# Performance work log

Measured on AMD Instinct MI355X. Metric: run time of the kernel, lower is better.

## Reference

```python
import jax, jax.numpy as jnp
import numpy as np

NTYPES = 2
NATOMS = (512, 512)
N = 1024          # total atoms
NN = 128          # neighbors per type
M = NTYPES * NN   # 256 neighbor slots per atom
D = 25            # last embedding width
FH = 240          # fitting hidden width
B = 8
RMIN, RMAX = 5.8, 6.0


def _embed_mlp(s, W0, b0, W1, b1, W2, b2):
    # DeepMD-style resnet embedding net: 1 -> D -> D -> D, tanh + skip
    h = jnp.tanh(s @ W0 + b0)
    h = h + jnp.tanh(h @ W1 + b1)
    h = h + jnp.tanh(h @ W2 + b2)
    return h


def setup_inputs() -> dict:
    key = jax.random.key(0)
    ks = jax.random.split(key, 20)
    # relative positions; components in [-4.5, 4.5] so |r| spans <5.8, [5.8,6.0), >=6.0
    image_dR = (jax.random.uniform(ks[0], (B, N, NTYPES, NN, 3), jnp.float32) - 0.5) * 9.0
    # 0 == empty neighbor slot (mask = list_neigh > 0); index-1 in [0, N)
    list_neigh = jax.random.randint(ks[1], (B, N, NTYPES, NN), 0, 1025)
    davg = 0.1 * jax.random.normal(ks[2], (NTYPES, M, 4), jnp.float32)
    dstd = jax.random.uniform(ks[3], (NTYPES, M, 4), jnp.float32, 0.5, 1.5)
    P = NTYPES * NTYPES
    eW0 = jax.random.normal(ks[4], (P, 1, D), jnp.float32)
    eb0 = 0.1 * jax.random.normal(ks[5], (P, D), jnp.float32)
    eW1 = jax.random.normal(ks[6], (P, D, D), jnp.float32) / np.sqrt(D)
    eb1 = 0.1 * jax.random.normal(ks[7], (P, D), jnp.float32)
    eW2 = jax.random.normal(ks[8], (P, D, D), jnp.float32) / np.sqrt(D)
    eb2 = 0.1 * jax.random.normal(ks[9], (P, D), jnp.float32)
    fW0 = jax.random.normal(ks[10], (NTYPES, 16 * D, FH), jnp.float32) / np.sqrt(16 * D)
    fb0 = 0.1 * jax.random.normal(ks[11], (NTYPES, FH), jnp.float32)
    fW1 = jax.random.normal(ks[12], (NTYPES, FH, FH), jnp.float32) / np.sqrt(FH)
    fb1 = 0.1 * jax.random.normal(ks[13], (NTYPES, FH), jnp.float32)
    fW2 = jax.random.normal(ks[14], (NTYPES, FH, FH), jnp.float32) / np.sqrt(FH)
    fb2 = 0.1 * jax.random.normal(ks[15], (NTYPES, FH), jnp.float32)
    fW3 = jax.random.normal(ks[16], (NTYPES, FH, 1), jnp.float32) / np.sqrt(FH)
    fb3 = 0.1 * jax.random.normal(ks[17], (NTYPES, 1), jnp.float32)
    ener_shift = 0.01 * jax.random.normal(ks[18], (NTYPES,), jnp.float32)
    return {
        'image_dR': image_dR, 'list_neigh': list_neigh,
        'davg': davg, 'dstd': dstd,
        'eW0': eW0, 'eb0': eb0, 'eW1': eW1, 'eb1': eb1, 'eW2': eW2, 'eb2': eb2,
        'fW0': fW0, 'fb0': fb0, 'fW1': fW1, 'fb1': fb1, 'fW2': fW2, 'fb2': fb2,
        'fW3': fW3, 'fb3': fb3, 'ener_shift': ener_shift,
        'dfeat': jnp.zeros((1,), jnp.float32),
        'Egroup_weight': jnp.zeros((1,), jnp.float32),
        'divider': jnp.ones((1,), jnp.float32),
    }


def _forward(image_dR, list_neigh, davg, dstd,
             eW0, eb0, eW1, eb1, eW2, eb2,
             fW0, fb0, fW1, fb1, fW2, fb2, fW3, fb3, ener_shift):
    dR = image_dR.reshape(B, N, M, 3)
    neigh = list_neigh.reshape(B, N, M)
    mask = neigh > 0
    mf = mask.astype(dR.dtype)
    dR2 = jnp.sum(dR * dR, axis=-1)                       # [B,N,M]
    safe_dR2 = jnp.where(mask, dR2, 1.0)
    Rij = jnp.sqrt(safe_dR2)
    inr = mf / Rij                                        # 1/|r|, 0 off-mask
    x = Rij * mf                                          # nr = dR2/Rij = |r|
    Ri_xyz = dR / safe_dR2[..., None] * mf[..., None]     # r / |r|^2
    inr2 = inr * inr
    inr4 = inr2 * inr2
    inr3 = inr4 * x
    # smooth switching function on [RMIN, RMAX]
    u = (x - RMIN) / (RMAX - RMIN)
    poly = u * u * u * (-6.0 * u * u + 15.0 * u - 10.0) + 1.0
    dpoly = (3.0 * u * u * (-6.0 * u * u + 15.0 * u - 10.0)
             + u * u * u * (-12.0 * u + 15.0)) / (RMAX - RMIN)
    mid = (x >= RMIN) & (x < RMAX)
    vv = jnp.where(x < RMIN, 1.0, jnp.where(mid, poly, 0.0)) * mf
    dvv = jnp.where(mid, dpoly, 0.0) * mf
    Ri_pre = jnp.concatenate([inr[..., None], Ri_xyz], axis=-1)   # [B,N,M,4]
    common = (dvv * inr)[..., None] * dR                          # [B,N,M,3]
    row0 = dR * (inr3 * vv)[..., None] - Ri_pre[..., 0:1] * common
    eye = jnp.eye(3, dtype=dR.dtype)
    outer = (2.0 * dR[..., :, None] * dR[..., None, :] * inr4[..., None, None]
             - eye * inr2[..., None, None])                       # [B,N,M,3,3]
    rows = outer * vv[..., None, None] - Ri_pre[..., 1:4, None] * common[..., None, :]
    Ri_d = jnp.concatenate([row0[..., None, :], rows], axis=-2) * mf[..., None, None]  # [B,N,M,4,3]
    Ri = Ri_pre * vv[..., None]
    # per-type normalization stats broadcast over atoms of each type
    davg_res = jnp.concatenate([jnp.broadcast_to(davg[t], (NATOMS[t], M, 4)) for t in range(NTYPES)], axis=0)
    dstd_res = jnp.concatenate([jnp.broadcast_to(dstd[t], (NATOMS[t], M, 4)) for t in range(NTYPES)], axis=0)
    Ri = (Ri - davg_res) / dstd_res
    Ri_d = Ri_d / dstd_res[..., None]

    def ei_fn(Ri_n):
        Ei_list = []
        start = 0
        for t in range(NTYPES):
            na = NATOMS[t]
            Rt = jax.lax.slice_in_dim(Ri_n, start, start + na, axis=1)  # [B,na,M,4]
            acc = jnp.zeros((B, na, 4, D), Ri_n.dtype)
            for t1 in range(NTYPES):
                p = t * NTYPES + t1
                blk = Rt[:, :, t1 * NN:(t1 + 1) * NN]                  # [B,na,NN,4]
                G = _embed_mlp(blk[..., 0:1], eW0[p], eb0[p], eW1[p], eb1[p], eW2[p], eb2[p])
                acc = acc + jnp.einsum('bnkd,bnke->bnde', blk, G)
            acc = acc * (4.0 / (NN * NTYPES * 4))
            DRt = jnp.einsum('bnde,bndf->bnef', acc, acc[..., :16]).reshape(B, na, D * 16)
            h = jnp.tanh(DRt @ fW0[t] + fb0[t])
            h = h + jnp.tanh(h @ fW1[t] + fb1[t])
            h = h + jnp.tanh(h @ fW2[t] + fb2[t])
            Ei_list.append(h @ fW3[t] + fb3[t] + ener_shift[t])
            start += na
        return jnp.concatenate(Ei_list, axis=1)   # [B,N,1]

    Ei, vjpf = jax.vjp(ei_fn, Ri)
    dE, = vjpf(jnp.ones_like(Ei))                 # dEi/dRi  [B,N,M,4]
    Etot = jnp.sum(Ei, axis=1)                    # [B,1]
    pair = jnp.einsum('bnmd,bnmdx->bnmx', dE, Ri_d)   # per-pair force term [B,N,M,3]
    F_self = -jnp.sum(pair, axis=2)
    j = neigh - 1
    valid = j >= 0
    flat_idx = jnp.where(valid, j, N) + jnp.arange(B)[:, None, None] * (N + 1)
    contrib = jnp.where(valid[..., None], pair, 0.0)
    seg = jax.ops.segment_sum(contrib.reshape(-1, 3), flat_idx.reshape(-1), num_segments=B * (N + 1))
    F = F_self + seg.reshape(B, N + 1, 3)[:, :N]
    return Etot, Ei, F


def reference(image_dR, list_neigh, davg, dstd,
              eW0, eb0, eW1, eb1, eW2, eb2,
              fW0, fb0, fW1, fb1, fW2, fb2, fW3, fb3, ener_shift,
              dfeat, Egroup_weight, divider):
    # dfeat / Egroup_weight / divider are in the torch forward signature but unused
    return _forward(image_dR, list_neigh, davg, dstd,
                    eW0, eb0, eW1, eb1, eW2, eb2,
                    fW0, fb0, fW1, fb1, fW2, fb2, fW3, fb3, ener_shift)
```

## Files before the change

kernel.cpp:

```cpp
#include <hip/hip_runtime.h>

#define DEV __device__ __forceinline__

namespace {

constexpr int B_ = 8;
constexpr int N_ = 1024;
constexpr int M_ = 256;
constexpr int D_ = 25;
constexpr int FH_ = 240;
constexpr int NATOM = B_ * N_;
constexpr float CSC = 1.0f / 256.0f;

DEV float fast_tanh(float x) {
  float ax = fabsf(x);
  float e = __expf(-2.0f * ax);
  float r = (1.0f - e) * __builtin_amdgcn_rcpf(1.0f + e);
  return copysignf(r, x);
}

template <bool WANT_RID>
DEV void compute_geom(float dx, float dy, float dz, int nb, int t, int m,
                      const float* __restrict__ davg, const float* __restrict__ dstd,
                      float* __restrict__ blk, float* __restrict__ rid) {
  float mf = (nb > 0) ? 1.0f : 0.0f;
  float dr2 = dx * dx + dy * dy + dz * dz;
  float safe = (nb > 0) ? dr2 : 1.0f;
  float rs = __builtin_amdgcn_rsqf(safe);
  float rij = safe * rs;
  float inr = mf * rs;
  float x = rij * mf;
  float inr2 = inr * inr;
  float inr4 = inr2 * inr2;
  float inr3 = inr4 * x;
  float u = (x - 5.8f) * 5.0f;
  float uu = u * u;
  float A = -6.0f * uu + 15.0f * u - 10.0f;
  float poly = uu * u * A + 1.0f;
  float dpoly = (3.0f * uu * A + uu * u * (-12.0f * u + 15.0f)) * 5.0f;
  bool mid = (x >= 5.8f) && (x < 6.0f);
  float vv = ((x < 5.8f) ? 1.0f : (mid ? poly : 0.0f)) * mf;
  float dvv = (mid ? dpoly : 0.0f) * mf;
  float pre[4];
  pre[0] = inr;
  pre[1] = dx * inr2;
  pre[2] = dy * inr2;
  pre[3] = dz * inr2;
  int bidx = (t * M_ + m) * 4;
  float4 av = *(const float4*)(davg + bidx);
  float4 sv = *(const float4*)(dstd + bidx);
  float avf[4] = {av.x, av.y, av.z, av.w};
  float rsv[4] = {__builtin_amdgcn_rcpf(sv.x), __builtin_amdgcn_rcpf(sv.y),
                  __builtin_amdgcn_rcpf(sv.z), __builtin_amdgcn_rcpf(sv.w)};
#pragma unroll
  for (int d = 0; d < 4; ++d) blk[d] = (pre[d] * vv - avf[d]) * rsv[d];
  if (WANT_RID) {
    float dv[3] = {dx, dy, dz};
    float ci = dvv * inr;
    float com[3];
#pragma unroll
    for (int c = 0; c < 3; ++c) com[c] = ci * dv[c];
    float iv = inr3 * vv;
#pragma unroll
    for (int c = 0; c < 3; ++c)
      rid[c] = (dv[c] * iv - pre[0] * com[c]) * mf * rsv[0];
#pragma unroll
    for (int r = 0; r < 3; ++r) {
#pragma unroll
      for (int c = 0; c < 3; ++c) {
        float outer = 2.0f * dv[r] * dv[c] * inr4 - ((r == c) ? inr2 : 0.0f);
        rid[(1 + r) * 3 + c] = (outer * vv - pre[1 + r] * com[c]) * mf * rsv[1 + r];
      }
    }
  }
}

DEV void embed_fwd(float s, const float* __restrict__ W0, const float* __restrict__ b0,
                   const float* __restrict__ W1, const float* __restrict__ b1,
                   const float* __restrict__ W2, const float* __restrict__ b2,
                   float* __restrict__ h0, float* __restrict__ t1v,
                   float* __restrict__ h1, float* __restrict__ t2v) {
#pragma unroll
  for (int e = 0; e < D_; ++e) h0[e] = fast_tanh(fmaf(s, W0[e], b0[e]));
  float a[D_];
#pragma unroll
  for (int e = 0; e < D_; ++e) a[e] = b1[e];
#pragma unroll
  for (int f = 0; f < D_; ++f) {
    float hf = h0[f];
#pragma unroll
    for (int e = 0; e < D_; ++e) a[e] = fmaf(hf, W1[f * D_ + e], a[e]);
  }
#pragma unroll
  for (int e = 0; e < D_; ++e) { t1v[e] = fast_tanh(a[e]); h1[e] = h0[e] + t1v[e]; }
#pragma unroll
  for (int e = 0; e < D_; ++e) a[e] = b2[e];
#pragma unroll
  for (int f = 0; f < D_; ++f) {
    float hf = h1[f];
#pragma unroll
    for (int e = 0; e < D_; ++e) a[e] = fmaf(hf, W2[f * D_ + e], a[e]);
  }
#pragma unroll
  for (int e = 0; e < D_; ++e) t2v[e] = fast_tanh(a[e]);
}

__global__ __launch_bounds__(256, 2) void k_embed_acc(
    const float* __restrict__ dR, const int* __restrict__ neigh,
    const float* __restrict__ davg, const float* __restrict__ dstd,
    const float* __restrict__ eW0, const float* __restrict__ eb0,
    const float* __restrict__ eW1, const float* __restrict__ eb1,
    const float* __restrict__ eW2, const float* __restrict__ eb2,
    float* __restrict__ acc_ws) {
  __shared__ float sG[M_ * D_];
  __shared__ float4 sBlk[M_];
  int atom = blockIdx.x;
  int n = atom & (N_ - 1);
  int t = (n >= 512) ? 1 : 0;
  int m = threadIdx.x;
  int p = __builtin_amdgcn_readfirstlane(t * 2 + (m >> 7));
  const float* W0 = eW0 + p * D_;
  const float* b0 = eb0 + p * D_;
  const float* W1 = eW1 + p * D_ * D_;
  const float* b1 = eb1 + p * D_;
  const float* W2 = eW2 + p * D_ * D_;
  const float* b2 = eb2 + p * D_;
  int base = atom * M_ + m;
  float dx = dR[base * 3 + 0];
  float dy = dR[base * 3 + 1];
  float dz = dR[base * 3 + 2];
  int nb = neigh[base];
  float blk[4];
  compute_geom<false>(dx, dy, dz, nb, t, m, davg, dstd, blk, nullptr);
  float h0[D_], t1v[D_], h1[D_], t2v[D_];
  embed_fwd(blk[0], W0, b0, W1, b1, W2, b2, h0, t1v, h1, t2v);
#pragma unroll
  for (int e = 0; e < D_; ++e) sG[m * D_ + e] = h1[e] + t2v[e];
  sBlk[m] = make_float4(blk[0], blk[1], blk[2], blk[3]);
  __syncthreads();
  if (threadIdx.x < 100) {
    int d = threadIdx.x & 3;
    int e = threadIdx.x >> 2;
    const float* sb = (const float*)sBlk;
    float sum = 0.0f;
    for (int mm = 0; mm < M_; ++mm)
      sum = fmaf(sb[mm * 4 + d], sG[mm * D_ + e], sum);
    acc_ws[atom * 100 + d * D_ + e] = sum * CSC;
  }
}

__global__ __launch_bounds__(256) void k_fit(
    const float* __restrict__ acc_ws,
    const float* __restrict__ fW0, const float* __restrict__ fb0,
    const float* __restrict__ fW1, const float* __restrict__ fb1,
    const float* __restrict__ fW2, const float* __restrict__ fb2,
    const float* __restrict__ fW3, const float* __restrict__ fb3,
    const float* __restrict__ ener_shift,
    float* __restrict__ dacc_ws, float* __restrict__ out) {
  constexpr int AB = 8;
  __shared__ float sAcc[AB][100];
  __shared__ float sX[AB][400];
  __shared__ float sH0[AB][FH_];
  __shared__ float sT1[AB][FH_];
  __shared__ float sH1[AB][FH_];
  __shared__ float sT2[AB][FH_];
  __shared__ float sEi[AB];
  int a0 = blockIdx.x * AB;
  int bb = a0 >> 10;
  int n0 = a0 & (N_ - 1);
  int t = (n0 >= 512) ? 1 : 0;
  int tid = threadIdx.x;
  for (int idx = tid; idx < AB * 100; idx += 256)
    ((float*)sAcc)[idx] = acc_ws[a0 * 100 + idx];
  if (tid < AB) sEi[tid] = 0.0f;
  __syncthreads();
  for (int idx = tid; idx < AB * 400; idx += 256) {
    int a = idx / 400; int r = idx % 400; int e = r >> 4; int f = r & 15;
    const float* A = sAcc[a];
    sX[a][r] = A[e] * A[f] + A[25 + e] * A[25 + f] + A[50 + e] * A[50 + f] +
               A[75 + e] * A[75 + f];
  }
  __syncthreads();
  const float* W0 = fW0 + t * 400 * FH_;
  const float* W1 = fW1 + t * FH_ * FH_;
  const float* W2 = fW2 + t * FH_ * FH_;
  const float* B0 = fb0 + t * FH_;
  const float* B1 = fb1 + t * FH_;
  const float* B2 = fb2 + t * FH_;
  const float* W3 = fW3 + t * FH_;
  int j = tid;
  if (j < FH_) {
    float acc8[AB];
#pragma unroll
    for (int a = 0; a < AB; ++a) acc8[a] = B0[j];
    for (int i = 0; i < 400; ++i) {
      float w = W0[i * FH_ + j];
#pragma unroll
      for (int a = 0; a < AB; ++a) acc8[a] = fmaf(sX[a][i], w, acc8[a]);
    }
#pragma unroll
    for (int a = 0; a < AB; ++a) sH0[a][j] = fast_tanh(acc8[a]);
  }
  __syncthreads();
  if (j < FH_) {
    float acc8[AB];
#pragma unroll
    for (int a = 0; a < AB; ++a) acc8[a] = B1[j];
    for (int f = 0; f < FH_; ++f) {
      float w = W1[f * FH_ + j];
#pragma unroll
      for (int a = 0; a < AB; ++a) acc8[a] = fmaf(sH0[a][f], w, acc8[a]);
    }
#pragma unroll
    for (int a = 0; a < AB; ++a) {
      float tv = fast_tanh(acc8[a]);
      sT1[a][j] = tv;
      sH1[a][j] = sH0[a][j] + tv;
    }
  }
  __syncthreads();
  if (j < FH_) {
    float acc8[AB];
#pragma unroll
    for (int a = 0; a < AB; ++a) acc8[a] = B2[j];
    for (int f = 0; f < FH_; ++f) {
      float w = W2[f * FH_ + j];
#pragma unroll
      for (int a = 0; a < AB; ++a) acc8[a] = fmaf(sH1[a][f], w, acc8[a]);
    }
    float w3 = W3[j];
#pragma unroll
    for (int a = 0; a < AB; ++a) {
      float tv = fast_tanh(acc8[a]);
      sT2[a][j] = tv;
      atomicAdd(&sEi[a], (sH1[a][j] + tv) * w3);
    }
  }
  __syncthreads();
  if (tid < AB) {
    float ei = sEi[tid] + fb3[t] + ener_shift[t];
    out[8 + a0 + tid] = ei;
    atomicAdd(&out[bb], ei);
  }
  if (j < FH_) {
    float w3 = W3[j];
#pragma unroll
    for (int a = 0; a < AB; ++a) {
      float tv = sT2[a][j];
      sT2[a][j] = w3 * (1.0f - tv * tv);
    }
  }
  __syncthreads();
  if (j < FH_) {
    float w3 = W3[j];
    float acc8[AB];
#pragma unroll
    for (int a = 0; a < AB; ++a) acc8[a] = w3;
    for (int k = 0; k < FH_; ++k) {
      float w = W2[j * FH_ + k];
#pragma unroll
      for (int a = 0; a < AB; ++a) acc8[a] = fmaf(sT2[a][k], w, acc8[a]);
    }
#pragma unroll
    for (int a = 0; a < AB; ++a) {
      float dh1 = acc8[a];
      float tv = sT1[a][j];
      sH1[a][j] = dh1;
      sT1[a][j] = dh1 * (1.0f - tv * tv);
    }
  }
  __syncthreads();
  if (j < FH_) {
    float acc8[AB];
#pragma unroll
    for (int a = 0; a < AB; ++a) acc8[a] = sH1[a][j];
    for (int k = 0; k < FH_; ++k) {
      float w = W1[j * FH_ + k];
#pragma unroll
      for (int a = 0; a < AB; ++a) acc8[a] = fmaf(sT1[a][k], w, acc8[a]);
    }
#pragma unroll
    for (int a = 0; a < AB; ++a) {
      float h0v = sH0[a][j];
      sH0[a][j] = acc8[a] * (1.0f - h0v * h0v);
    }
  }
  __syncthreads();
  for (int i = tid; i < 400; i += 256) {
    float acc8[AB];
#pragma unroll
    for (int a = 0; a < AB; ++a) acc8[a] = 0.0f;
    for (int jj = 0; jj < FH_; ++jj) {
      float w = W0[i * FH_ + jj];
#pragma unroll
      for (int a = 0; a < AB; ++a) acc8[a] = fmaf(sH0[a][jj], w, acc8[a]);
    }
#pragma unroll
    for (int a = 0; a < AB; ++a) sX[a][i] = acc8[a];
  }
  __syncthreads();
  for (int idx = tid; idx < AB * 100; idx += 256) {
    int a = idx / 100; int r = idx % 100; int d = r / 25; int e = r % 25;
    const float* A = sAcc[a];
    const float* DX = sX[a];
    float sum = 0.0f;
#pragma unroll
    for (int f = 0; f < 16; ++f) sum = fmaf(DX[e * 16 + f], A[d * 25 + f], sum);
    if (e < 16) {
#pragma unroll
      for (int e2 = 0; e2 < 25; ++e2) sum = fmaf(DX[e2 * 16 + e], A[d * 25 + e2], sum);
    }
    dacc_ws[a0 * 100 + idx] = sum;
  }
}

__global__ __launch_bounds__(256, 2) void k_bwd_force(
    const float* __restrict__ dR, const int* __restrict__ neigh,
    const float* __restrict__ davg, const float* __restrict__ dstd,
    const float* __restrict__ eW0, const float* __restrict__ eb0,
    const float* __restrict__ eW1, const float* __restrict__ eb1,
    const float* __restrict__ eW2, const float* __restrict__ eb2,
    const float* __restrict__ dacc_ws, float* __restrict__ out) {
  __shared__ float sF[3];
  int atom = blockIdx.x;
  int bb = atom >> 10;
  int n = atom & (N_ - 1);
  int t = (n >= 512) ? 1 : 0;
  int m = threadIdx.x;
  if (m < 3) sF[m] = 0.0f;
  __syncthreads();
  int p = __builtin_amdgcn_readfirstlane(t * 2 + (m >> 7));
  const float* W0 = eW0 + p * D_;
  const float* b0 = eb0 + p * D_;
  const float* W1 = eW1 + p * D_ * D_;
  const float* b1 = eb1 + p * D_;
  const float* W2 = eW2 + p * D_ * D_;
  const float* b2 = eb2 + p * D_;
  const float* dac = dacc_ws + atom * 100;
  int base = atom * M_ + m;
  float dx = dR[base * 3 + 0];
  float dy = dR[base * 3 + 1];
  float dz = dR[base * 3 + 2];
  int nb = neigh[base];
  float blk[4], rid[12];
  compute_geom<true>(dx, dy, dz, nb, t, m, davg, dstd, blk, rid);
  float h0[D_], t1v[D_], h1[D_], t2v[D_];
  embed_fwd(blk[0], W0, b0, W1, b1, W2, b2, h0, t1v, h1, t2v);
  float dblk[4];
#pragma unroll
  for (int d = 0; d < 4; ++d) {
    float s = 0.0f;
#pragma unroll
    for (int e = 0; e < D_; ++e) s = fmaf(dac[d * D_ + e], h1[e] + t2v[e], s);
    dblk[d] = s * CSC;
  }
  float dG[D_];
#pragma unroll
  for (int e = 0; e < D_; ++e)
    dG[e] = CSC * (dac[e] * blk[0] + dac[25 + e] * blk[1] +
                   dac[50 + e] * blk[2] + dac[75 + e] * blk[3]);
  float g[D_];
#pragma unroll
  for (int e = 0; e < D_; ++e) g[e] = dG[e] * (1.0f - t2v[e] * t2v[e]);
#pragma unroll
  for (int e = 0; e < D_; ++e) {
    float s = dG[e];
#pragma unroll
    for (int f = 0; f < D_; ++f) s = fmaf(g[f], W2[e * D_ + f], s);
    dG[e] = s;
  }
#pragma unroll
  for (int e = 0; e < D_; ++e) g[e] = dG[e] * (1.0f - t1v[e] * t1v[e]);
#pragma unroll
  for (int e = 0; e < D_; ++e) {
    float s = dG[e];
#pragma unroll
    for (int f = 0; f < D_; ++f) s = fmaf(g[f], W1[e * D_ + f], s);
    dG[e] = s;
  }
  float ds = 0.0f;
#pragma unroll
  for (int e = 0; e < D_; ++e) ds = fmaf(dG[e] * (1.0f - h0[e] * h0[e]), W0[e], ds);
  float dE0 = dblk[0] + ds, dE1 = dblk[1], dE2 = dblk[2], dE3 = dblk[3];
  float px = dE0 * rid[0] + dE1 * rid[3] + dE2 * rid[6] + dE3 * rid[9];
  float py = dE0 * rid[1] + dE1 * rid[4] + dE2 * rid[7] + dE3 * rid[10];
  float pz = dE0 * rid[2] + dE1 * rid[5] + dE2 * rid[8] + dE3 * rid[11];
  atomicAdd(&sF[0], px);
  atomicAdd(&sF[1], py);
  atomicAdd(&sF[2], pz);
  if (nb > 0) {
    int jn = nb - 1;
    int fi = 8 + NATOM + (bb * N_ + jn) * 3;
    atomicAdd(&out[fi + 0], px);
    atomicAdd(&out[fi + 1], py);
    atomicAdd(&out[fi + 2], pz);
  }
  __syncthreads();
  if (m < 3) atomicAdd(&out[8 + NATOM + atom * 3 + m], -sF[m]);
}

}

extern "C" void kernel_launch(void* const* d_in, const int* in_sizes, int n_in,
                              void* d_out, int out_size, void* d_ws, size_t ws_size,
                              hipStream_t stream) {
  (void)in_sizes; (void)n_in; (void)ws_size;
  const float* image_dR   = (const float*)d_in[0];
  const int*   list_neigh = (const int*)d_in[1];
  const float* davg       = (const float*)d_in[2];
  const float* dstd       = (const float*)d_in[3];
  const float* eW0        = (const float*)d_in[4];
  const float* eb0        = (const float*)d_in[5];
  const float* eW1        = (const float*)d_in[6];
  const float* eb1        = (const float*)d_in[7];
  const float* eW2        = (const float*)d_in[8];
  const float* eb2        = (const float*)d_in[9];
  const float* fW0        = (const float*)d_in[10];
  const float* fb0        = (const float*)d_in[11];
  const float* fW1        = (const float*)d_in[12];
  const float* fb1        = (const float*)d_in[13];
  const float* fW2        = (const float*)d_in[14];
  const float* fb2        = (const float*)d_in[15];
  const float* fW3        = (const float*)d_in[16];
  const float* fb3        = (const float*)d_in[17];
  const float* ener_shift = (const float*)d_in[18];
  float* out = (float*)d_out;
  float* acc_ws  = (float*)d_ws;
  float* dacc_ws = acc_ws + NATOM * 100;

  hipMemsetAsync(d_out, 0, (size_t)out_size * sizeof(float), stream);
  k_embed_acc<<<NATOM, 256, 0, stream>>>(image_dR, list_neigh, davg, dstd,
                                         eW0, eb0, eW1, eb1, eW2, eb2, acc_ws);
  k_fit<<<NATOM / 8, 256, 0, stream>>>(acc_ws, fW0, fb0, fW1, fb1, fW2, fb2,
                                       fW3, fb3, ener_shift, dacc_ws, out);
  k_bwd_force<<<NATOM, 256, 0, stream>>>(image_dR, list_neigh, davg, dstd,
                                         eW0, eb0, eW1, eb1, eW2, eb2,
                                         dacc_ws, out);
}
```

Baseline: 1.081 ms.

## Replace embedding-net backward with forward-mode tangent propagation and wave-shuffle force reduction

```diff
diff --git a/kernel.cpp b/kernel.cpp
--- a/kernel.cpp
+++ b/kernel.cpp
@@ -19,93 +19,51 @@
   return copysignf(r, x);
 }
 
-template <bool WANT_RID>
-DEV void compute_geom(float dx, float dy, float dz, int nb, int t, int m,
-                      const float* __restrict__ davg, const float* __restrict__ dstd,
-                      float* __restrict__ blk, float* __restrict__ rid) {
-  float mf = (nb > 0) ? 1.0f : 0.0f;
+struct Geom {
+  float mf, inr, inr2, inr4, inr3, vv, dvv;
+};
+
+DEV Geom geom_core(float dx, float dy, float dz, int nb) {
+  Geom g;
+  g.mf = (nb > 0) ? 1.0f : 0.0f;
   float dr2 = dx * dx + dy * dy + dz * dz;
   float safe = (nb > 0) ? dr2 : 1.0f;
   float rs = __builtin_amdgcn_rsqf(safe);
   float rij = safe * rs;
-  float inr = mf * rs;
-  float x = rij * mf;
-  float inr2 = inr * inr;
-  float inr4 = inr2 * inr2;
-  float inr3 = inr4 * x;
+  g.inr = g.mf * rs;
+  float x = rij * g.mf;
+  g.inr2 = g.inr * g.inr;
+  g.inr4 = g.inr2 * g.inr2;
+  g.inr3 = g.inr4 * x;
   float u = (x - 5.8f) * 5.0f;
   float uu = u * u;
   float A = -6.0f * uu + 15.0f * u - 10.0f;
   float poly = uu * u * A + 1.0f;
   float dpoly = (3.0f * uu * A + uu * u * (-12.0f * u + 15.0f)) * 5.0f;
   bool mid = (x >= 5.8f) && (x < 6.0f);
-  float vv = ((x < 5.8f) ? 1.0f : (mid ? poly : 0.0f)) * mf;
-  float dvv = (mid ? dpoly : 0.0f) * mf;
-  float pre[4];
-  pre[0] = inr;
-  pre[1] = dx * inr2;
-  pre[2] = dy * inr2;
-  pre[3] = dz * inr2;
+  g.vv = ((x < 5.8f) ? 1.0f : (mid ? poly : 0.0f)) * g.mf;
+  g.dvv = (mid ? dpoly : 0.0f) * g.mf;
+  return g;
+}
+
+DEV void geom_blk(const Geom& g, float dx, float dy, float dz, int t, int m,
+                  const float* __restrict__ davg, const float* __restrict__ dstd,
+                  float* __restrict__ blk, float* __restrict__ rsv) {
   int bidx = (t * M_ + m) * 4;
   float4 av = *(const float4*)(davg + bidx);
   float4 sv = *(const float4*)(dstd + bidx);
+  float pre[4] = {g.inr, dx * g.inr2, dy * g.inr2, dz * g.inr2};
   float avf[4] = {av.x, av.y, av.z, av.w};
-  float rsv[4] = {__builtin_amdgcn_rcpf(sv.x), __builtin_amdgcn_rcpf(sv.y),
-                  __builtin_amdgcn_rcpf(sv.z), __builtin_amdgcn_rcpf(sv.w)};
-#pragma unroll
-  for (int d = 0; d < 4; ++d) blk[d] = (pre[d] * vv - avf[d]) * rsv[d];
-  if (WANT_RID) {
-    float dv[3] = {dx, dy, dz};
-    float ci = dvv * inr;
-    float com[3];
-#pragma unroll
-    for (int c = 0; c < 3; ++c) com[c] = ci * dv[c];
-    float iv = inr3 * vv;
-#pragma unroll
-    for (int c = 0; c < 3; ++c)
-      rid[c] = (dv[c] * iv - pre[0] * com[c]) * mf * rsv[0];
-#pragma unroll
-    for (int r = 0; r < 3; ++r) {
-#pragma unroll
-      for (int c = 0; c < 3; ++c) {
-        float outer = 2.0f * dv[r] * dv[c] * inr4 - ((r == c) ? inr2 : 0.0f);
-        rid[(1 + r) * 3 + c] = (outer * vv - pre[1 + r] * com[c]) * mf * rsv[1 + r];
-      }
-    }
-  }
-}
-
-DEV void embed_fwd(float s, const float* __restrict__ W0, const float* __restrict__ b0,
-                   const float* __restrict__ W1, const float* __restrict__ b1,
-                   const float* __restrict__ W2, const float* __restrict__ b2,
-                   float* __restrict__ h0, float* __restrict__ t1v,
-                   float* __restrict__ h1, float* __restrict__ t2v) {
-#pragma unroll
-  for (int e = 0; e < D_; ++e) h0[e] = fast_tanh(fmaf(s, W0[e], b0[e]));
-  float a[D_];
-#pragma unroll
-  for (int e = 0; e < D_; ++e) a[e] = b1[e];
-#pragma unroll
-  for (int f = 0; f < D_; ++f) {
-    float hf = h0[f];
-#pragma unroll
-    for (int e = 0; e < D_; ++e) a[e] = fmaf(hf, W1[f * D_ + e], a[e]);
-  }
-#pragma unroll
-  for (int e = 0; e < D_; ++e) { t1v[e] = fast_tanh(a[e]); h1[e] = h0[e] + t1v[e]; }
-#pragma unroll
-  for (int e = 0; e < D_; ++e) a[e] = b2[e];
-#pragma unroll
-  for (int f = 0; f < D_; ++f) {
-    float hf = h1[f];
-#pragma unroll
-    for (int e = 0; e < D_; ++e) a[e] = fmaf(hf, W2[f * D_ + e], a[e]);
-  }
-#pragma unroll
-  for (int e = 0; e < D_; ++e) t2v[e] = fast_tanh(a[e]);
-}
-
-__global__ __launch_bounds__(256, 2) void k_embed_acc(
+  float svf[4] = {sv.x, sv.y, sv.z, sv.w};
+#pragma unroll
+  for (int d = 0; d < 4; ++d) {
+    rsv[d] = __builtin_amdgcn_rcpf(svf[d]);
+    blk[d] = (pre[d] * g.vv - avf[d]) * rsv[d];
+  }
+}
+
+__global__ __launch_bounds__(256) __attribute__((amdgpu_waves_per_eu(2, 4)))
+void k_embed_acc(
     const float* __restrict__ dR, const int* __restrict__ neigh,
     const float* __restrict__ davg, const float* __restrict__ dstd,
     const float* __restrict__ eW0, const float* __restrict__ eb0,
@@ -130,12 +88,33 @@
   float dy = dR[base * 3 + 1];
   float dz = dR[base * 3 + 2];
   int nb = neigh[base];
-  float blk[4];
-  compute_geom<false>(dx, dy, dz, nb, t, m, davg, dstd, blk, nullptr);
-  float h0[D_], t1v[D_], h1[D_], t2v[D_];
-  embed_fwd(blk[0], W0, b0, W1, b1, W2, b2, h0, t1v, h1, t2v);
-#pragma unroll
-  for (int e = 0; e < D_; ++e) sG[m * D_ + e] = h1[e] + t2v[e];
+  Geom g = geom_core(dx, dy, dz, nb);
+  float blk[4], rsv[4];
+  geom_blk(g, dx, dy, dz, t, m, davg, dstd, blk, rsv);
+  float s = blk[0];
+  float h[D_], a[D_];
+#pragma unroll
+  for (int e = 0; e < D_; ++e) h[e] = fast_tanh(fmaf(s, W0[e], b0[e]));
+#pragma unroll
+  for (int e = 0; e < D_; ++e) a[e] = b1[e];
+#pragma unroll
+  for (int f = 0; f < D_; ++f) {
+    float hf = h[f];
+#pragma unroll
+    for (int e = 0; e < D_; ++e) a[e] = fmaf(hf, W1[f * D_ + e], a[e]);
+  }
+#pragma unroll
+  for (int e = 0; e < D_; ++e) h[e] += fast_tanh(a[e]);
+#pragma unroll
+  for (int e = 0; e < D_; ++e) a[e] = b2[e];
+#pragma unroll
+  for (int f = 0; f < D_; ++f) {
+    float hf = h[f];
+#pragma unroll
+    for (int e = 0; e < D_; ++e) a[e] = fmaf(hf, W2[f * D_ + e], a[e]);
+  }
+#pragma unroll
+  for (int e = 0; e < D_; ++e) sG[m * D_ + e] = h[e] + fast_tanh(a[e]);
   sBlk[m] = make_float4(blk[0], blk[1], blk[2], blk[3]);
   __syncthreads();
   if (threadIdx.x < 100) {
@@ -314,21 +293,19 @@
   }
 }
 
-__global__ __launch_bounds__(256, 2) void k_bwd_force(
+__global__ __launch_bounds__(256) __attribute__((amdgpu_waves_per_eu(2, 2)))
+void k_bwd_force(
     const float* __restrict__ dR, const int* __restrict__ neigh,
     const float* __restrict__ davg, const float* __restrict__ dstd,
     const float* __restrict__ eW0, const float* __restrict__ eb0,
     const float* __restrict__ eW1, const float* __restrict__ eb1,
     const float* __restrict__ eW2, const float* __restrict__ eb2,
     const float* __restrict__ dacc_ws, float* __restrict__ out) {
-  __shared__ float sF[3];
   int atom = blockIdx.x;
   int bb = atom >> 10;
   int n = atom & (N_ - 1);
   int t = (n >= 512) ? 1 : 0;
   int m = threadIdx.x;
-  if (m < 3) sF[m] = 0.0f;
-  __syncthreads();
   int p = __builtin_amdgcn_readfirstlane(t * 2 + (m >> 7));
   const float* W0 = eW0 + p * D_;
   const float* b0 = eb0 + p * D_;
@@ -342,52 +319,99 @@
   float dy = dR[base * 3 + 1];
   float dz = dR[base * 3 + 2];
   int nb = neigh[base];
-  float blk[4], rid[12];
-  compute_geom<true>(dx, dy, dz, nb, t, m, davg, dstd, blk, rid);
-  float h0[D_], t1v[D_], h1[D_], t2v[D_];
-  embed_fwd(blk[0], W0, b0, W1, b1, W2, b2, h0, t1v, h1, t2v);
-  float dblk[4];
-#pragma unroll
-  for (int d = 0; d < 4; ++d) {
-    float s = 0.0f;
-#pragma unroll
-    for (int e = 0; e < D_; ++e) s = fmaf(dac[d * D_ + e], h1[e] + t2v[e], s);
-    dblk[d] = s * CSC;
-  }
-  float dG[D_];
-#pragma unroll
-  for (int e = 0; e < D_; ++e)
-    dG[e] = CSC * (dac[e] * blk[0] + dac[25 + e] * blk[1] +
-                   dac[50 + e] * blk[2] + dac[75 + e] * blk[3]);
-  float g[D_];
-#pragma unroll
-  for (int e = 0; e < D_; ++e) g[e] = dG[e] * (1.0f - t2v[e] * t2v[e]);
+  Geom g = geom_core(dx, dy, dz, nb);
+  float blk[4], rsv[4];
+  geom_blk(g, dx, dy, dz, t, m, davg, dstd, blk, rsv);
+
+  float s = blk[0];
+  float h[D_], hp[D_];
 #pragma unroll
   for (int e = 0; e < D_; ++e) {
-    float s = dG[e];
-#pragma unroll
-    for (int f = 0; f < D_; ++f) s = fmaf(g[f], W2[e * D_ + f], s);
-    dG[e] = s;
-  }
-#pragma unroll
-  for (int e = 0; e < D_; ++e) g[e] = dG[e] * (1.0f - t1v[e] * t1v[e]);
+    float th = fast_tanh(fmaf(s, W0[e], b0[e]));
+    h[e] = th;
+    hp[e] = (1.0f - th * th) * W0[e];
+  }
+  {
+    float a[D_], ap[D_];
+#pragma unroll
+    for (int e = 0; e < D_; ++e) { a[e] = b1[e]; ap[e] = 0.0f; }
+#pragma unroll
+    for (int f = 0; f < D_; ++f) {
+      float hf = h[f], gf = hp[f];
+#pragma unroll
+      for (int e = 0; e < D_; ++e) {
+        float w = W1[f * D_ + e];
+        a[e] = fmaf(hf, w, a[e]);
+        ap[e] = fmaf(gf, w, ap[e]);
+      }
+    }
+#pragma unroll
+    for (int e = 0; e < D_; ++e) {
+      float th = fast_tanh(a[e]);
+      h[e] += th;
+      hp[e] = fmaf(1.0f - th * th, ap[e], hp[e]);
+    }
+  }
+  {
+    float a[D_], ap[D_];
+#pragma unroll
+    for (int e = 0; e < D_; ++e) { a[e] = b2[e]; ap[e] = 0.0f; }
+#pragma unroll
+    for (int f = 0; f < D_; ++f) {
+      float hf = h[f], gf = hp[f];
+#pragma unroll
+      for (int e = 0; e < D_; ++e) {
+        float w = W2[f * D_ + e];
+        a[e] = fmaf(hf, w, a[e]);
+        ap[e] = fmaf(gf, w, ap[e]);
+      }
+    }
+#pragma unroll
+    for (int e = 0; e < D_; ++e) {
+      float th = fast_tanh(a[e]);
+      h[e] += th;
+      hp[e] = fmaf(1.0f - th * th, ap[e], hp[e]);
+    }
+  }
+
+  float ds = 0.0f, db0 = 0.0f, db1 = 0.0f, db2 = 0.0f, db3 = 0.0f;
 #pragma unroll
   for (int e = 0; e < D_; ++e) {
-    float s = dG[e];
-#pragma unroll
-    for (int f = 0; f < D_; ++f) s = fmaf(g[f], W1[e * D_ + f], s);
-    dG[e] = s;
-  }
-  float ds = 0.0f;
-#pragma unroll
-  for (int e = 0; e < D_; ++e) ds = fmaf(dG[e] * (1.0f - h0[e] * h0[e]), W0[e], ds);
-  float dE0 = dblk[0] + ds, dE1 = dblk[1], dE2 = dblk[2], dE3 = dblk[3];
-  float px = dE0 * rid[0] + dE1 * rid[3] + dE2 * rid[6] + dE3 * rid[9];
-  float py = dE0 * rid[1] + dE1 * rid[4] + dE2 * rid[7] + dE3 * rid[10];
-  float pz = dE0 * rid[2] + dE1 * rid[5] + dE2 * rid[8] + dE3 * rid[11];
-  atomicAdd(&sF[0], px);
-  atomicAdd(&sF[1], py);
-  atomicAdd(&sF[2], pz);
+    float d0 = dac[e], d1 = dac[25 + e], d2 = dac[50 + e], d3 = dac[75 + e];
+    float gG = d0 * blk[0] + d1 * blk[1] + d2 * blk[2] + d3 * blk[3];
+    ds = fmaf(gG, hp[e], ds);
+    float he = h[e];
+    db0 = fmaf(d0, he, db0);
+    db1 = fmaf(d1, he, db1);
+    db2 = fmaf(d2, he, db2);
+    db3 = fmaf(d3, he, db3);
+  }
+  float dE0 = (db0 + ds) * CSC;
+  float dE1 = db1 * CSC, dE2 = db2 * CSC, dE3 = db3 * CSC;
+
+  float dv[3] = {dx, dy, dz};
+  float pre1[3] = {dx * g.inr2, dy * g.inr2, dz * g.inr2};
+  float ci = g.dvv * g.inr;
+  float com[3];
+#pragma unroll
+  for (int c = 0; c < 3; ++c) com[c] = ci * dv[c];
+  float iv = g.inr3 * g.vv;
+  float pc[3];
+  float f0 = dE0 * rsv[0];
+#pragma unroll
+  for (int c = 0; c < 3; ++c) pc[c] = f0 * (dv[c] * iv - g.inr * com[c]);
+  float dEr[3] = {dE1, dE2, dE3};
+#pragma unroll
+  for (int r = 0; r < 3; ++r) {
+    float fr = dEr[r] * rsv[1 + r];
+#pragma unroll
+    for (int c = 0; c < 3; ++c) {
+      float outer = 2.0f * dv[r] * dv[c] * g.inr4 - ((r == c) ? g.inr2 : 0.0f);
+      pc[c] = fmaf(fr, outer * g.vv - pre1[r] * com[c], pc[c]);
+    }
+  }
+  float px = pc[0] * g.mf, py = pc[1] * g.mf, pz = pc[2] * g.mf;
+
   if (nb > 0) {
     int jn = nb - 1;
     int fi = 8 + NATOM + (bb * N_ + jn) * 3;
@@ -395,8 +419,18 @@
     atomicAdd(&out[fi + 1], py);
     atomicAdd(&out[fi + 2], pz);
   }
-  __syncthreads();
-  if (m < 3) atomicAdd(&out[8 + NATOM + atom * 3 + m], -sF[m]);
+#pragma unroll
+  for (int i = 1; i < 64; i <<= 1) {
+    px += __shfl_xor(px, i);
+    py += __shfl_xor(py, i);
+    pz += __shfl_xor(pz, i);
+  }
+  if ((m & 63) == 0) {
+    int fi = 8 + NATOM + atom * 3;
+    atomicAdd(&out[fi + 0], -px);
+    atomicAdd(&out[fi + 1], -py);
+    atomicAdd(&out[fi + 2], -pz);
+  }
 }
 
 }
```

Result: faster. 973.1 us (-10.0%).
